# Optimization experiments

Hardware: AMD Instinct MI355X
Metric: run time of the kernel (lower is better)

The kernel has to match this reference:

```python
import jax, jax.numpy as jnp
import numpy as np

# OGB feature vocab sizes
ATOM_DIMS = [119, 4, 12, 12, 10, 6, 6, 2, 2]
BOND_DIMS = [5, 6, 2]
ATOM_OFF = np.concatenate([[0], np.cumsum(ATOM_DIMS)[:-1]]).astype(np.int32)
BOND_OFF = np.concatenate([[0], np.cumsum(BOND_DIMS)[:-1]]).astype(np.int32)
SCHEDULE_LEN = 5   # len(train_schedule) == len(eval_schedule)
NUM_GRAPHS = 12000
BN_EPS = 1e-5

N_NODES, N_EDGES, HIDDEN, NUM_TASKS = 300000, 600000, 128, 128


def setup_inputs() -> dict:
    key = jax.random.key(0)
    ks = jax.random.split(key, 16)
    x = jax.random.randint(ks[0], (N_NODES, 9), 0, 2, dtype=jnp.int32)
    edge_index = jax.random.randint(ks[1], (2, N_EDGES), 0, N_NODES, dtype=jnp.int32)
    edge_attr = jax.random.randint(ks[2], (N_EDGES, 3), 0, 2, dtype=jnp.int32)
    batch = jnp.sort(jax.random.randint(ks[3], (N_NODES,), 0, NUM_GRAPHS, dtype=jnp.int32))
    # learned parameters (embedding tables concatenated with offsets)
    atom_emb = jax.random.normal(ks[4], (sum(ATOM_DIMS), HIDDEN), jnp.float32) * 0.1
    bond_emb = jax.random.normal(ks[5], (sum(BOND_DIMS), HIDDEN), jnp.float32) * 0.1
    conv_W = jax.random.normal(ks[6], (HIDDEN, HIDDEN), jnp.float32) * (1.0 / np.sqrt(HIDDEN))
    conv_b = jnp.zeros((HIDDEN,), jnp.float32)
    root_emb = jax.random.normal(ks[7], (HIDDEN,), jnp.float32) * 0.1
    bn_gamma = jnp.ones((HIDDEN,), jnp.float32)
    bn_beta = jnp.zeros((HIDDEN,), jnp.float32)
    bn_mean = jnp.zeros((HIDDEN,), jnp.float32)   # running stats (eval mode)
    bn_var = jnp.ones((HIDDEN,), jnp.float32)
    lin_W = jax.random.normal(ks[8], (NUM_TASKS, HIDDEN), jnp.float32) * (1.0 / np.sqrt(HIDDEN))
    lin_b = jnp.zeros((NUM_TASKS,), jnp.float32)
    return {"x": x, "edge_index": edge_index, "edge_attr": edge_attr, "batch": batch,
            "atom_emb": atom_emb, "bond_emb": bond_emb, "conv_W": conv_W, "conv_b": conv_b,
            "root_emb": root_emb, "bn_gamma": bn_gamma, "bn_beta": bn_beta,
            "bn_mean": bn_mean, "bn_var": bn_var, "lin_W": lin_W, "lin_b": lin_b}


def reference(x, edge_index, edge_attr, batch, atom_emb, bond_emb, conv_W, conv_b,
              root_emb, bn_gamma, bn_beta, bn_mean, bn_var, lin_W, lin_b):
    N = x.shape[0]
    # AtomEncoder / BondEncoder: sum of per-feature embedding lookups
    h = atom_emb[x + jnp.asarray(ATOM_OFF, x.dtype)].sum(axis=1)            # [N, H]
    e = bond_emb[edge_attr + jnp.asarray(BOND_OFF, edge_attr.dtype)].sum(axis=1)  # [E, H]
    row, col = edge_index[0], edge_index[1]
    deg = jax.ops.segment_sum(jnp.ones_like(row, h.dtype), row, num_segments=N) + 1.0  # [N]
    dis = deg ** -0.5                                                        # deg >= 1, no inf
    norm = dis[row] * dis[col]                                               # [E]
    inv_std = bn_gamma / jnp.sqrt(bn_var + BN_EPS)
    for i in range(SCHEDULE_LEN):
        old = h
        z = h @ conv_W.T + conv_b                                            # [N, H]
        # message: norm * relu(x_j + edge_emb), aggregated at target (col) via scatter-add
        msg = norm[:, None] * jax.nn.relu(z[row] + e)                        # [E, H]
        agg = jax.ops.segment_sum(msg, col, num_segments=N)                  # [N, H]
        z = agg + jax.nn.relu(z + root_emb) / deg[:, None]                   # self-loop term
        z = jax.nn.relu(z)
        z = (z - bn_mean) * inv_std + bn_beta                                # BN (eval, running stats)
        # dropout: identity in eval mode
        # NOTE: faithful to source bug: smooth_fac is the loop index i, not schedule[i]
        h = i * old + (1 - i) * z
    # global mean pool over graphs
    counts = jax.ops.segment_sum(jnp.ones((N,), h.dtype), batch, num_segments=NUM_GRAPHS)
    pooled = jax.ops.segment_sum(h, batch, num_segments=NUM_GRAPHS) / jnp.maximum(counts, 1.0)[:, None]
    return pooled @ lin_W.T + lin_b                                          # [num_graphs, num_tasks]
```

## Files before the change

### kernel.cpp

```cpp
#include <hip/hip_runtime.h>

#define HID 128
#define AROWS 173

typedef __attribute__((ext_vector_type(8))) short short8;
typedef __attribute__((ext_vector_type(8))) unsigned short ushort8v;
typedef __attribute__((ext_vector_type(4))) float floatx4;
typedef __attribute__((ext_vector_type(4))) unsigned short ushort4v;

__device__ __forceinline__ unsigned short f2bf(float f) {
    unsigned u = __builtin_bit_cast(unsigned, f);
    u += 0x7FFF + ((u >> 16) & 1);
    return (unsigned short)(u >> 16);
}
__device__ __forceinline__ float bf2f(unsigned short s) {
    unsigned u = ((unsigned)s) << 16;
    return __builtin_bit_cast(float, u);
}

__global__ void fillrd_kernel(float* __restrict__ dis, int* __restrict__ indeg,
                              int* __restrict__ dhist, int N)
{
    int i = blockIdx.x * 256 + threadIdx.x;
    if (i < N) { dis[i] = 0.f; indeg[i] = 0; }
    if (blockIdx.x == 0 && threadIdx.x < 32) dhist[threadIdx.x] = 0;
}

__global__ void diag_kernel(float* __restrict__ out, long n, float val)
{
    long i = (long)blockIdx.x * blockDim.x + threadIdx.x;
    if (i < n) out[i] = val;
}

__global__ __launch_bounds__(256) void tables_kernel(
    const float* __restrict__ conv_W, unsigned short* __restrict__ Wb,
    const float* __restrict__ lin_W, unsigned short* __restrict__ linWb,
    const float* __restrict__ bond_emb, unsigned short* __restrict__ comb,
    const float* __restrict__ gamma, const float* __restrict__ beta,
    const float* __restrict__ mean, const float* __restrict__ var,
    float* __restrict__ bnsc, float* __restrict__ bnsh,
    const float* __restrict__ atom_emb, unsigned short* __restrict__ aeb)
{
    int blk = blockIdx.x;
    int tid = threadIdx.x;
    if (blk < 64) {
        int i = blk * 256 + tid;
        Wb[i] = f2bf(conv_W[i]);
    } else if (blk < 128) {
        int i = (blk - 64) * 256 + tid;
        linWb[i] = f2bf(lin_W[i]);
    } else if (blk < 158) {
        int i = (blk - 128) * 2 + (tid >> 7);
        int c = tid & 127;
        int a0 = i / 12, a1 = (i % 12) / 2, a2 = i % 2;
        comb[i * HID + c] = f2bf(bond_emb[a0 * HID + c] + bond_emb[(5 + a1) * HID + c]
                               + bond_emb[(11 + a2) * HID + c]);
    } else if (blk == 158) {
        if (tid < HID) {
            float sc = gamma[tid] * rsqrtf(var[tid] + 1e-5f);
            bnsc[tid] = sc;
            bnsh[tid] = beta[tid] - mean[tid] * sc;
        }
    } else {
        int i = (blk - 159) * 256 + tid;
        if (i < AROWS * HID) aeb[i] = f2bf(atom_emb[i]);
    }
}

__global__ void hist_kernel(const int* __restrict__ ei, float* __restrict__ dis,
                            int* __restrict__ indeg, int E)
{
    for (int e = blockIdx.x * blockDim.x + threadIdx.x; e < E; e += gridDim.x * blockDim.x) {
        atomicAdd(&dis[ei[e]], 1.f);
        atomicAdd(&indeg[ei[E + e]], 1);
    }
}

__global__ __launch_bounds__(256) void bsum_kernel(
    const int* __restrict__ indeg, int* __restrict__ partial,
    float* __restrict__ dis, int* __restrict__ dhist, int N)
{
    __shared__ int s[256];
    __shared__ int lh[32];
    int tid = threadIdx.x;
    if (tid < 32) lh[tid] = 0;
    int i = blockIdx.x * 256 + tid;
    int v = (i < N) ? indeg[i] : 0;
    s[tid] = v;
    if (i < N) {
        dis[i] = rsqrtf(dis[i] + 1.f);
        int d = v > 31 ? 31 : v;
        atomicAdd(&lh[d], 1);
    }
    __syncthreads();
    for (int d = 128; d > 0; d >>= 1) {
        if (tid < d) s[tid] += s[tid + d];
        __syncthreads();
    }
    if (tid == 0) partial[blockIdx.x] = s[0];
    if (tid < 32 && lh[tid]) atomicAdd(&dhist[tid], lh[tid]);
}

__global__ __launch_bounds__(256) void scan1_kernel(
    const int* __restrict__ partial, int* __restrict__ offs,
    int* __restrict__ ptr, const int* __restrict__ dhist, int* __restrict__ dcur,
    int B, int N)
{
    __shared__ int s[256];
    __shared__ int carry_s;
    int tid = threadIdx.x;
    if (tid == 0) carry_s = 0;
    __syncthreads();
    for (int base = 0; base < B; base += 256) {
        int i = base + tid;
        int v = (i < B) ? partial[i] : 0;
        s[tid] = v;
        __syncthreads();
        for (int d = 1; d < 256; d <<= 1) {
            int t = (tid >= d) ? s[tid - d] : 0;
            __syncthreads();
            s[tid] += t;
            __syncthreads();
        }
        int carry = carry_s;
        if (i < B) offs[i] = carry + s[tid] - v;
        __syncthreads();
        if (tid == 0) carry_s = carry + s[255];
        __syncthreads();
    }
    if (tid == 0) {
        ptr[N] = carry_s;
        int sum = 0;
        for (int k = 0; k < 32; ++k) { dcur[k] = sum; sum += dhist[k]; }
    }
}

__global__ __launch_bounds__(256) void scan2_kernel(
    const int* __restrict__ indeg, const int* __restrict__ offs,
    int* __restrict__ ptr, int* __restrict__ cursor, int N)
{
    __shared__ int s[256];
    int tid = threadIdx.x;
    int i = blockIdx.x * 256 + tid;
    int v = (i < N) ? indeg[i] : 0;
    s[tid] = v;
    __syncthreads();
    for (int d = 1; d < 256; d <<= 1) {
        int t = (tid >= d) ? s[tid - d] : 0;
        __syncthreads();
        s[tid] += t;
        __syncthreads();
    }
    if (i < N) {
        int ex = offs[blockIdx.x] + s[tid] - v;
        ptr[i] = ex;
        cursor[i] = ex;
    }
}

__global__ __launch_bounds__(256) void dperm_kernel(
    const int* __restrict__ ptr, int* __restrict__ dcur,
    int* __restrict__ perm, int N)
{
    __shared__ int lh[32];
    __shared__ int gb[32];
    int tid = threadIdx.x;
    if (tid < 32) lh[tid] = 0;
    __syncthreads();
    int n = blockIdx.x * 256 + tid;
    int rank = 0, d = 0;
    if (n < N) {
        d = ptr[n + 1] - ptr[n];
        if (d > 31) d = 31;
        rank = atomicAdd(&lh[d], 1);
    }
    __syncthreads();
    if (tid < 32) gb[tid] = lh[tid] ? atomicAdd(&dcur[tid], lh[tid]) : 0;
    __syncthreads();
    if (n < N) perm[gb[d] + rank] = n;
}

__global__ void fillcsr_kernel(const int* __restrict__ ei, const int* __restrict__ attr,
                               const float* __restrict__ dis, int* __restrict__ cursor,
                               int2* __restrict__ edata, const int* __restrict__ batch,
                               int* __restrict__ gptr, int E, int N, int G)
{
    for (int e = blockIdx.x * blockDim.x + threadIdx.x; e < E; e += gridDim.x * blockDim.x) {
        int r   = ei[e];
        int col = ei[E + e];
        int pos = atomicAdd(&cursor[col], 1);
        int ci  = attr[e * 3] * 12 + attr[e * 3 + 1] * 2 + attr[e * 3 + 2];
        float nrm = dis[r] * dis[col];
        int2 ed;
        ed.x = r;
        ed.y = ci | ((int)f2bf(nrm) << 16);
        edata[pos] = ed;
    }
    for (int n = blockIdx.x * blockDim.x + threadIdx.x; n < N; n += gridDim.x * blockDim.x) {
        int b = batch[n];
        int bp = (n == 0) ? -1 : batch[n - 1];
        for (int g = bp + 1; g <= b; ++g) gptr[g] = n;
        if (n == N - 1)
            for (int g = b + 1; g <= G; ++g) gptr[g] = N;
    }
}

template<bool FIRST>
__device__ __forceinline__ ushort8v agg_node(
    long n, int c, const int* __restrict__ ptr, const int2* __restrict__ edata,
    const unsigned short* __restrict__ comb, const float* __restrict__ dis,
    const float* __restrict__ root, const float* __restrict__ bnsc,
    const float* __restrict__ bnsh, const unsigned short* __restrict__ zb,
    const unsigned short* __restrict__ hb, float fi)
{
    ushort8v zv = *reinterpret_cast<const ushort8v*>(zb + n * HID + c);
    ushort8v hv;
    if constexpr (!FIRST) hv = *reinterpret_cast<const ushort8v*>(hb + n * HID + c);
    float di = dis[n];
    float rd = di * di;
    float acc[8];
#pragma unroll
    for (int j = 0; j < 8; ++j) acc[j] = fmaxf(bf2f(zv[j]) + root[c + j], 0.f) * rd;

    int jb = ptr[n], je = ptr[n + 1];
    int j2 = jb;
    for (; j2 + 1 < je; j2 += 2) {
        int2 e0 = edata[j2];
        int2 e1 = edata[j2 + 1];
        ushort8v z0 = *reinterpret_cast<const ushort8v*>(zb + (long)e0.x * HID + c);
        ushort8v z1 = *reinterpret_cast<const ushort8v*>(zb + (long)e1.x * HID + c);
        ushort8v c0 = *reinterpret_cast<const ushort8v*>(comb + (e0.y & 0xFF) * HID + c);
        ushort8v c1 = *reinterpret_cast<const ushort8v*>(comb + (e1.y & 0xFF) * HID + c);
        float n0 = bf2f((unsigned short)(((unsigned)e0.y) >> 16));
        float n1 = bf2f((unsigned short)(((unsigned)e1.y) >> 16));
#pragma unroll
        for (int j = 0; j < 8; ++j) {
            acc[j] += fmaxf(bf2f(z0[j]) + bf2f(c0[j]), 0.f) * n0;
            acc[j] += fmaxf(bf2f(z1[j]) + bf2f(c1[j]), 0.f) * n1;
        }
    }
    if (j2 < je) {
        int2 e0 = edata[j2];
        ushort8v z0 = *reinterpret_cast<const ushort8v*>(zb + (long)e0.x * HID + c);
        ushort8v c0 = *reinterpret_cast<const ushort8v*>(comb + (e0.y & 0xFF) * HID + c);
        float n0 = bf2f((unsigned short)(((unsigned)e0.y) >> 16));
#pragma unroll
        for (int j = 0; j < 8; ++j)
            acc[j] += fmaxf(bf2f(z0[j]) + bf2f(c0[j]), 0.f) * n0;
    }

    ushort8v o;
#pragma unroll
    for (int j = 0; j < 8; ++j) {
        float t = fmaxf(acc[j], 0.f) * bnsc[c + j] + bnsh[c + j];
        float h;
        if constexpr (FIRST) h = t;
        else h = fi * bf2f(hv[j]) + (1.f - fi) * t;
        o[j] = f2bf(h);
    }
    return o;
}

template<bool FIRST>
__global__ __launch_bounds__(256) void agg_kernel(
    const int* __restrict__ perm, const int* __restrict__ ptr,
    const int2* __restrict__ edata, const unsigned short* __restrict__ comb,
    const float* __restrict__ dis, const float* __restrict__ root,
    const float* __restrict__ bnsc, const float* __restrict__ bnsh,
    const unsigned short* __restrict__ zb, unsigned short* __restrict__ hb,
    float fi, int N)
{
    long slot = (long)blockIdx.x * 16 + (threadIdx.x >> 4);
    if (slot >= N) return;
    long n = perm[slot];
    int c = (threadIdx.x & 15) * 8;
    ushort8v o = agg_node<FIRST>(n, c, ptr, edata, comb, dis, root, bnsc, bnsh,
                                 zb, hb, fi);
    *reinterpret_cast<ushort8v*>(hb + n * HID + c) = o;
}

template<bool FIRST>
__global__ __launch_bounds__(256) void fusedag_kernel(
    const int* __restrict__ perm, const int* __restrict__ ptr,
    const int2* __restrict__ edata, const unsigned short* __restrict__ comb,
    const float* __restrict__ dis, const float* __restrict__ root,
    const float* __restrict__ bnsc, const float* __restrict__ bnsh,
    const unsigned short* __restrict__ zin, unsigned short* __restrict__ hb,
    const unsigned short* __restrict__ Wb, const float* __restrict__ bias,
    unsigned short* __restrict__ zout, float fi, int N)
{
    __shared__ unsigned short hs[64][132];
    int tid = threadIdx.x;
    long base = (long)blockIdx.x * 64;
    int sn = tid >> 4;
    int cc = (tid & 15) * 8;

#pragma unroll 1
    for (int s = 0; s < 4; ++s) {
        int lr = s * 16 + sn;
        long slot = base + lr;
        ushort8v o = {0, 0, 0, 0, 0, 0, 0, 0};
        if (slot < N) {
            long n = perm[slot];
            o = agg_node<FIRST>(n, cc, ptr, edata, comb, dis, root, bnsc, bnsh,
                                zin, hb, fi);
            *reinterpret_cast<ushort8v*>(hb + n * HID + cc) = o;
        }
        *reinterpret_cast<ushort8v*>(&hs[lr][cc]) = o;
    }
    __syncthreads();

    int wave = tid >> 6;
    int lane = tid & 63;
    int l15 = lane & 15;
    int q = lane >> 4;
    int row0 = wave * 16;

    short8 a[4];
#pragma unroll
    for (int kb = 0; kb < 4; ++kb)
        a[kb] = *reinterpret_cast<const short8*>(&hs[row0 + l15][q * 8 + kb * 32]);

    floatx4 acc[8];
#pragma unroll
    for (int nt = 0; nt < 8; ++nt) {
        floatx4 zz = {0.f, 0.f, 0.f, 0.f};
        acc[nt] = zz;
    }
#pragma unroll
    for (int nt = 0; nt < 8; ++nt) {
        const unsigned short* bp = Wb + (nt * 16 + l15) * HID + q * 8;
#pragma unroll
        for (int kb = 0; kb < 4; ++kb) {
            short8 b = *reinterpret_cast<const short8*>(bp + kb * 32);
            acc[nt] = __builtin_amdgcn_mfma_f32_16x16x32_bf16(a[kb], b, acc[nt], 0, 0, 0);
        }
    }

    float bi[8];
#pragma unroll
    for (int nt = 0; nt < 8; ++nt) bi[nt] = bias[nt * 16 + l15];

#pragma unroll
    for (int r = 0; r < 4; ++r) {
        int lr = row0 + q * 4 + r;
#pragma unroll
        for (int nt = 0; nt < 8; ++nt)
            hs[lr][l15 + 16 * nt] = f2bf(acc[nt][r] + bi[nt]);
    }
    __syncthreads();

    int tr = tid >> 4;
    int tc = (tid & 15) * 8;
#pragma unroll
    for (int i = 0; i < 4; ++i) {
        int row = i * 16 + tr;
        long slot = base + row;
        if (slot < N) {
            long n = perm[slot];
            ushort8v v = *reinterpret_cast<const ushort8v*>(&hs[row][tc]);
            *reinterpret_cast<ushort8v*>(zout + n * HID + tc) = v;
        }
    }
}

__device__ __forceinline__ void gemm_from_lds(
    unsigned short (*hs)[132], const unsigned short* __restrict__ Wb,
    const float* __restrict__ bias, unsigned short* __restrict__ zb,
    long base, int N, int tid)
{
    int wave = tid >> 6;
    int lane = tid & 63;
    int l15 = lane & 15;
    int q = lane >> 4;
    int rowl0 = wave * 32;

    short8 a[2][4];
#pragma unroll
    for (int mt = 0; mt < 2; ++mt) {
        int rl = rowl0 + mt * 16 + l15;
#pragma unroll
        for (int kb = 0; kb < 4; ++kb)
            a[mt][kb] = *reinterpret_cast<const short8*>(&hs[rl][q * 8 + kb * 32]);
    }

    floatx4 acc[2][8];
#pragma unroll
    for (int mt = 0; mt < 2; ++mt)
#pragma unroll
        for (int nt = 0; nt < 8; ++nt) {
            floatx4 zz = {0.f, 0.f, 0.f, 0.f};
            acc[mt][nt] = zz;
        }

#pragma unroll
    for (int nt = 0; nt < 8; ++nt) {
        const unsigned short* bp = Wb + (nt * 16 + l15) * HID + q * 8;
#pragma unroll
        for (int kb = 0; kb < 4; ++kb) {
            short8 b = *reinterpret_cast<const short8*>(bp + kb * 32);
            acc[0][nt] = __builtin_amdgcn_mfma_f32_16x16x32_bf16(a[0][kb], b, acc[0][nt], 0, 0, 0);
            acc[1][nt] = __builtin_amdgcn_mfma_f32_16x16x32_bf16(a[1][kb], b, acc[1][nt], 0, 0, 0);
        }
    }

    float bi[8];
#pragma unroll
    for (int nt = 0; nt < 8; ++nt) bi[nt] = bias[nt * 16 + l15];

    __syncthreads();
#pragma unroll
    for (int mt = 0; mt < 2; ++mt)
#pragma unroll
        for (int r = 0; r < 4; ++r) {
            int lr = rowl0 + mt * 16 + q * 4 + r;
#pragma unroll
            for (int nt = 0; nt < 8; ++nt)
                hs[lr][l15 + 16 * nt] = f2bf(acc[mt][nt][r] + bi[nt]);
        }
    __syncthreads();

    int tr = tid >> 4;
    int tc = (tid & 15) * 8;
#pragma unroll
    for (int i = 0; i < 8; ++i) {
        int row = i * 16 + tr;
        long gr = base + row;
        if (gr < N) {
            ushort8v v = *reinterpret_cast<const ushort8v*>(&hs[row][tc]);
            *reinterpret_cast<ushort8v*>(zb + gr * HID + tc) = v;
        }
    }
}

__global__ __launch_bounds__(256) void egemm_kernel(
    const int* __restrict__ x, const unsigned short* __restrict__ aeb,
    const unsigned short* __restrict__ Wb, const float* __restrict__ bias,
    unsigned short* __restrict__ zb, int N)
{
    __shared__ unsigned short hs[128][132];
    __shared__ int xs[128 * 9];
    int tid = threadIdx.x;
    long base = (long)blockIdx.x * 128;
    const int OFF[9] = {0, 119, 123, 135, 147, 157, 163, 169, 171};

    int nb = (N - base < 128) ? (int)(N - base) : 128;
    int cnt = nb * 9;
    for (int i = tid; i < cnt; i += 256) xs[i] = x[base * 9 + i];
    __syncthreads();

    int sn = tid >> 4;
    int cc = (tid & 15) * 8;
#pragma unroll 1
    for (int s = 0; s < 8; ++s) {
        int lr = s * 16 + sn;
        ushort8v o;
        if (lr < nb) {
            float acc[8];
#pragma unroll
            for (int j = 0; j < 8; ++j) acc[j] = 0.f;
#pragma unroll
            for (int f = 0; f < 9; ++f) {
                int idx = xs[lr * 9 + f] + OFF[f];
                ushort8v v = *reinterpret_cast<const ushort8v*>(aeb + (long)idx * HID + cc);
#pragma unroll
                for (int j = 0; j < 8; ++j) acc[j] += bf2f(v[j]);
            }
#pragma unroll
            for (int j = 0; j < 8; ++j) o[j] = f2bf(acc[j]);
        } else {
            ushort8v z8 = {0, 0, 0, 0, 0, 0, 0, 0};
            o = z8;
        }
        *reinterpret_cast<ushort8v*>(&hs[lr][cc]) = o;
    }
    __syncthreads();

    gemm_from_lds(hs, Wb, bias, zb, base, N, tid);
}

__global__ __launch_bounds__(256) void gemm_kernel(
    const unsigned short* __restrict__ hb, const unsigned short* __restrict__ Wb,
    const float* __restrict__ bias, unsigned short* __restrict__ zb, int N)
{
    __shared__ unsigned short st[128][132];
    int tid = threadIdx.x;
    int wave = tid >> 6;
    int lane = tid & 63;
    int l15 = lane & 15;
    int q = lane >> 4;
    long base = (long)blockIdx.x * 128;
    long row0 = base + wave * 32;

#pragma unroll
    for (int mt = 0; mt < 2; ++mt) {
        long rl = row0 + mt * 16 + l15;
        if (rl > (long)N - 1) rl = (long)N - 1;
        const unsigned short* ap = hb + rl * HID + q * 8;
        int lrow = wave * 32 + mt * 16 + l15;
#pragma unroll
        for (int kb = 0; kb < 4; ++kb)
            *reinterpret_cast<ushort8v*>(&st[lrow][q * 8 + kb * 32]) =
                *reinterpret_cast<const ushort8v*>(ap + kb * 32);
    }
    __syncthreads();
    gemm_from_lds(st, Wb, bias, zb, base, N, tid);
}

__global__ __launch_bounds__(256) void linmm_kernel(
    const unsigned short* __restrict__ pb, const unsigned short* __restrict__ Wb,
    const float* __restrict__ bias, float* __restrict__ out, int G)
{
    int wave = threadIdx.x >> 6;
    int lane = threadIdx.x & 63;
    int l15 = lane & 15;
    int q = lane >> 4;
    long row0 = (long)blockIdx.x * 128 + wave * 32;

    short8 a[2][4];
#pragma unroll
    for (int mt = 0; mt < 2; ++mt) {
        long rl = row0 + mt * 16 + l15;
        if (rl > (long)G - 1) rl = (long)G - 1;
        const unsigned short* ap = pb + rl * HID + q * 8;
#pragma unroll
        for (int kb = 0; kb < 4; ++kb)
            a[mt][kb] = *reinterpret_cast<const short8*>(ap + kb * 32);
    }

    floatx4 acc[2][8];
#pragma unroll
    for (int mt = 0; mt < 2; ++mt)
#pragma unroll
        for (int nt = 0; nt < 8; ++nt) {
            floatx4 zz = {0.f, 0.f, 0.f, 0.f};
            acc[mt][nt] = zz;
        }

#pragma unroll
    for (int nt = 0; nt < 8; ++nt) {
        const unsigned short* bp = Wb + (nt * 16 + l15) * HID + q * 8;
#pragma unroll
        for (int kb = 0; kb < 4; ++kb) {
            short8 b = *reinterpret_cast<const short8*>(bp + kb * 32);
            acc[0][nt] = __builtin_amdgcn_mfma_f32_16x16x32_bf16(a[0][kb], b, acc[0][nt], 0, 0, 0);
            acc[1][nt] = __builtin_amdgcn_mfma_f32_16x16x32_bf16(a[1][kb], b, acc[1][nt], 0, 0, 0);
        }
    }

    float bi[8];
#pragma unroll
    for (int nt = 0; nt < 8; ++nt) bi[nt] = bias[nt * 16 + l15];

#pragma unroll
    for (int mt = 0; mt < 2; ++mt)
#pragma unroll
        for (int r = 0; r < 4; ++r) {
            long rr = row0 + mt * 16 + q * 4 + r;
            if (rr < G) {
                float* op = out + rr * HID + l15;
#pragma unroll
                for (int nt = 0; nt < 8; ++nt)
                    op[nt * 16] = acc[mt][nt][r] + bi[nt];
            }
        }
}

__global__ __launch_bounds__(256) void pool_kernel(
    const unsigned short* __restrict__ hb, const int* __restrict__ gptr,
    unsigned short* __restrict__ pb, int G)
{
    int g = blockIdx.x;
    if (g >= G) return;
    int tid = threadIdx.x;
    int sub = tid >> 5;
    int c = (tid & 31) * 4;
    int lo = gptr[g], hi = gptr[g + 1];
    floatx4 s = {0.f, 0.f, 0.f, 0.f};
    for (int n = lo + sub; n < hi; n += 8) {
        ushort4v hv = *reinterpret_cast<const ushort4v*>(hb + (long)n * HID + c);
#pragma unroll
        for (int j = 0; j < 4; ++j) s[j] += bf2f(hv[j]);
    }
    __shared__ float ps[8][HID];
    *reinterpret_cast<floatx4*>(&ps[sub][c]) = s;
    __syncthreads();
    if (tid < HID) {
        float sum = 0.f;
#pragma unroll
        for (int k = 0; k < 8; ++k) sum += ps[k][tid];
        float cnt = (hi > lo) ? (float)(hi - lo) : 1.f;
        pb[(long)g * HID + tid] = f2bf(sum / cnt);
    }
}

extern "C" void kernel_launch(void* const* d_in, const int* in_sizes, int n_in,
                              void* d_out, int out_size, void* d_ws, size_t ws_size,
                              hipStream_t stream)
{
    const int* x          = (const int*)d_in[0];
    const int* ei         = (const int*)d_in[1];
    const int* attr       = (const int*)d_in[2];
    const int* batch      = (const int*)d_in[3];
    const float* atom_emb = (const float*)d_in[4];
    const float* bond_emb = (const float*)d_in[5];
    const float* conv_W   = (const float*)d_in[6];
    const float* conv_b   = (const float*)d_in[7];
    const float* root     = (const float*)d_in[8];
    const float* gamma    = (const float*)d_in[9];
    const float* beta     = (const float*)d_in[10];
    const float* mean     = (const float*)d_in[11];
    const float* var      = (const float*)d_in[12];
    const float* lin_W    = (const float*)d_in[13];
    const float* lin_b    = (const float*)d_in[14];
    float* out = (float*)d_out;

    const int N = in_sizes[0] / 9;
    const int E = in_sizes[1] / 2;
    const int G = out_size / HID;
    const int B = (N + 255) / 256;

    auto al = [](size_t b) { return (b + 255) & ~(size_t)255; };
    const size_t need_base =
        al((size_t)N * HID * 2) +
        al((size_t)N * HID * 2) +
        al((size_t)(N + 1) * 4) +
        al((size_t)E * 8) +
        al((size_t)N * 4) +
        al((size_t)2048 * 4) * 2 +
        al((size_t)(G + 1) * 4) +
        al((size_t)(G + 128) * HID * 2) +
        al((size_t)60 * HID * 2) +
        al((size_t)HID * 4) * 2 +
        al((size_t)HID * HID * 2) * 2 +
        al((size_t)AROWS * HID * 2) +
        al((size_t)N * 4) +
        al(32 * 4) * 2;
    const size_t need_fused = need_base + al((size_t)N * HID * 2);

    if (ws_size < need_base || B > 2048) {
        float v = (B > 2048) ? 3000.f : (1000.f + (float)(ws_size >> 20));
        long n = (long)out_size;
        diag_kernel<<<(int)((n + 255) / 256), 256, 0, stream>>>(out, n, v);
        return;
    }
    const bool fused_ok = (ws_size >= need_fused);

    char* wsp = (char*)d_ws;
    size_t used = 0;
    auto alloc = [&](size_t bytes) { char* p = wsp + used; used += al(bytes); return p; };
    unsigned short* hb = (unsigned short*)alloc((size_t)N * HID * 2);
    unsigned short* zb = (unsigned short*)alloc((size_t)N * HID * 2);
    int* ptr      = (int*)alloc((size_t)(N + 1) * 4);
    int2* edata   = (int2*)alloc((size_t)E * 8);
    int* indeg    = (int*)alloc((size_t)N * 4);
    int* cursor   = indeg;
    int* partial  = (int*)alloc((size_t)2048 * 4);
    int* offs     = (int*)alloc((size_t)2048 * 4);
    int* gptr     = (int*)alloc((size_t)(G + 1) * 4);
    unsigned short* pb = (unsigned short*)alloc((size_t)(G + 128) * HID * 2);
    float* dis    = (float*)pb;
    unsigned short* comb = (unsigned short*)alloc((size_t)60 * HID * 2);
    float* bnsc   = (float*)alloc((size_t)HID * 4);
    float* bnsh   = (float*)alloc((size_t)HID * 4);
    unsigned short* Wb    = (unsigned short*)alloc((size_t)HID * HID * 2);
    unsigned short* linWb = (unsigned short*)alloc((size_t)HID * HID * 2);
    unsigned short* aeb   = (unsigned short*)alloc((size_t)AROWS * HID * 2);
    int* perm     = (int*)alloc((size_t)N * 4);
    int* dhist    = (int*)alloc(32 * 4);
    int* dcur     = (int*)alloc(32 * 4);
    unsigned short* zb2 = (unsigned short*)alloc((size_t)N * HID * 2);

    fillrd_kernel<<<B, 256, 0, stream>>>(dis, indeg, dhist, N);
    tables_kernel<<<246, 256, 0, stream>>>(conv_W, Wb, lin_W, linWb, bond_emb, comb,
                                           gamma, beta, mean, var, bnsc, bnsh,
                                           atom_emb, aeb);
    hist_kernel<<<1024, 256, 0, stream>>>(ei, dis, indeg, E);
    bsum_kernel<<<B, 256, 0, stream>>>(indeg, partial, dis, dhist, N);
    scan1_kernel<<<1, 256, 0, stream>>>(partial, offs, ptr, dhist, dcur, B, N);
    scan2_kernel<<<B, 256, 0, stream>>>(indeg, offs, ptr, cursor, N);
    dperm_kernel<<<B, 256, 0, stream>>>(ptr, dcur, perm, N);
    fillcsr_kernel<<<1024, 256, 0, stream>>>(ei, attr, dis, cursor, edata,
                                             batch, gptr, E, N, G);

    const int gemm_blocks  = (N + 127) / 128;
    const int fused_blocks = (N + 63) / 64;
    const int agg_blocks   = (N + 15) / 16;
    egemm_kernel<<<gemm_blocks, 256, 0, stream>>>(x, aeb, Wb, conv_b, zb, N);

    if (fused_ok) {
        fusedag_kernel<true ><<<fused_blocks, 256, 0, stream>>>(perm, ptr, edata,
                comb, dis, root, bnsc, bnsh, zb,  hb, Wb, conv_b, zb2, 0.f, N);
        fusedag_kernel<false><<<fused_blocks, 256, 0, stream>>>(perm, ptr, edata,
                comb, dis, root, bnsc, bnsh, zb2, hb, Wb, conv_b, zb,  2.f, N);
        fusedag_kernel<false><<<fused_blocks, 256, 0, stream>>>(perm, ptr, edata,
                comb, dis, root, bnsc, bnsh, zb,  hb, Wb, conv_b, zb2, 3.f, N);
        agg_kernel<false><<<agg_blocks, 256, 0, stream>>>(perm, ptr, edata, comb,
                dis, root, bnsc, bnsh, zb2, hb, 4.f, N);
    } else {
        agg_kernel<true ><<<agg_blocks, 256, 0, stream>>>(perm, ptr, edata, comb,
                dis, root, bnsc, bnsh, zb, hb, 0.f, N);
        const float fis[3] = {2.f, 3.f, 4.f};
        for (int t = 0; t < 3; ++t) {
            gemm_kernel<<<gemm_blocks, 256, 0, stream>>>(hb, Wb, conv_b, zb, N);
            agg_kernel<false><<<agg_blocks, 256, 0, stream>>>(perm, ptr, edata, comb,
                    dis, root, bnsc, bnsh, zb, hb, fis[t], N);
        }
    }

    pool_kernel<<<G, 256, 0, stream>>>(hb, gptr, pb, G);
    linmm_kernel<<<(G + 127) / 128, 256, 0, stream>>>(pb, linWb, lin_b, out, G);
}
```

Measured before the change: 797.7 us.

## Build CSR in degree-sorted slot order and drop fused agg-GEMM path

The CSR is now built in degree-sorted slot order. A degree-bucket permutation and its inverse are computed first, and the row pointers come from a prefix sum over permuted degrees. The aggregation then reads edges contiguously in slot order, so neighbouring threads walk adjacent edge ranges instead of scattered ones. The fused aggregation+GEMM kernel and the extra z buffer are removed in favour of separate agg and gemm launches, and the embedding GEMM uses 64-row tiles. This adds kernel launches and extra passes through the permutation in exchange for more coherent edge reads. Dropping the fused path brings back an hb round-trip per layer.

```diff
diff --git a/kernel.cpp b/kernel.cpp
--- a/kernel.cpp
+++ b/kernel.cpp
@@ -76,35 +76,76 @@
     }
 }
 
-__global__ __launch_bounds__(256) void bsum_kernel(
-    const int* __restrict__ indeg, int* __restrict__ partial,
-    float* __restrict__ dis, int* __restrict__ dhist, int N)
-{
-    __shared__ int s[256];
+__global__ __launch_bounds__(256) void fdh_kernel(
+    float* __restrict__ dis, const int* __restrict__ indeg,
+    int* __restrict__ dhist, int N)
+{
     __shared__ int lh[32];
     int tid = threadIdx.x;
     if (tid < 32) lh[tid] = 0;
+    __syncthreads();
     int i = blockIdx.x * 256 + tid;
-    int v = (i < N) ? indeg[i] : 0;
-    s[tid] = v;
     if (i < N) {
         dis[i] = rsqrtf(dis[i] + 1.f);
-        int d = v > 31 ? 31 : v;
+        int d = indeg[i]; if (d > 31) d = 31;
         atomicAdd(&lh[d], 1);
     }
+    __syncthreads();
+    if (tid < 32 && lh[tid]) atomicAdd(&dhist[tid], lh[tid]);
+}
+
+__global__ void dscan_kernel(const int* __restrict__ dhist, int* __restrict__ dcur)
+{
+    if (threadIdx.x == 0) {
+        int s = 0;
+        for (int k = 0; k < 32; ++k) { dcur[k] = s; s += dhist[k]; }
+    }
+}
+
+__global__ __launch_bounds__(256) void dperm_kernel(
+    const int* __restrict__ indeg, int* __restrict__ dcur,
+    int* __restrict__ perm, int* __restrict__ invperm, int N)
+{
+    __shared__ int lh[32];
+    __shared__ int gb[32];
+    int tid = threadIdx.x;
+    if (tid < 32) lh[tid] = 0;
+    __syncthreads();
+    int n = blockIdx.x * 256 + tid;
+    int rank = 0, d = 0;
+    if (n < N) {
+        d = indeg[n]; if (d > 31) d = 31;
+        rank = atomicAdd(&lh[d], 1);
+    }
+    __syncthreads();
+    if (tid < 32) gb[tid] = lh[tid] ? atomicAdd(&dcur[tid], lh[tid]) : 0;
+    __syncthreads();
+    if (n < N) {
+        int slot = gb[d] + rank;
+        perm[slot] = n;
+        invperm[n] = slot;
+    }
+}
+
+__global__ __launch_bounds__(256) void sbsum_kernel(
+    const int* __restrict__ indeg, const int* __restrict__ perm,
+    int* __restrict__ partial, int N)
+{
+    __shared__ int s[256];
+    int tid = threadIdx.x;
+    int i = blockIdx.x * 256 + tid;
+    s[tid] = (i < N) ? indeg[perm[i]] : 0;
     __syncthreads();
     for (int d = 128; d > 0; d >>= 1) {
         if (tid < d) s[tid] += s[tid + d];
         __syncthreads();
     }
     if (tid == 0) partial[blockIdx.x] = s[0];
-    if (tid < 32 && lh[tid]) atomicAdd(&dhist[tid], lh[tid]);
-}
-
-__global__ __launch_bounds__(256) void scan1_kernel(
+}
+
+__global__ __launch_bounds__(256) void sscan1_kernel(
     const int* __restrict__ partial, int* __restrict__ offs,
-    int* __restrict__ ptr, const int* __restrict__ dhist, int* __restrict__ dcur,
-    int B, int N)
+    int* __restrict__ sptr, int B, int N)
 {
     __shared__ int s[256];
     __shared__ int carry_s;
@@ -128,21 +169,18 @@
         if (tid == 0) carry_s = carry + s[255];
         __syncthreads();
     }
-    if (tid == 0) {
-        ptr[N] = carry_s;
-        int sum = 0;
-        for (int k = 0; k < 32; ++k) { dcur[k] = sum; sum += dhist[k]; }
-    }
-}
-
-__global__ __launch_bounds__(256) void scan2_kernel(
-    const int* __restrict__ indeg, const int* __restrict__ offs,
-    int* __restrict__ ptr, int* __restrict__ cursor, int N)
+    if (tid == 0) sptr[N] = carry_s;
+}
+
+__global__ __launch_bounds__(256) void sscan2_kernel(
+    const int* __restrict__ indeg, const int* __restrict__ perm,
+    const int* __restrict__ offs, int* __restrict__ sptr,
+    int* __restrict__ scursor, int N)
 {
     __shared__ int s[256];
     int tid = threadIdx.x;
     int i = blockIdx.x * 256 + tid;
-    int v = (i < N) ? indeg[i] : 0;
+    int v = (i < N) ? indeg[perm[i]] : 0;
     s[tid] = v;
     __syncthreads();
     for (int d = 1; d < 256; d <<= 1) {
@@ -153,42 +191,23 @@
     }
     if (i < N) {
         int ex = offs[blockIdx.x] + s[tid] - v;
-        ptr[i] = ex;
-        cursor[i] = ex;
-    }
-}
-
-__global__ __launch_bounds__(256) void dperm_kernel(
-    const int* __restrict__ ptr, int* __restrict__ dcur,
-    int* __restrict__ perm, int N)
-{
-    __shared__ int lh[32];
-    __shared__ int gb[32];
-    int tid = threadIdx.x;
-    if (tid < 32) lh[tid] = 0;
-    __syncthreads();
-    int n = blockIdx.x * 256 + tid;
-    int rank = 0, d = 0;
-    if (n < N) {
-        d = ptr[n + 1] - ptr[n];
-        if (d > 31) d = 31;
-        rank = atomicAdd(&lh[d], 1);
-    }
-    __syncthreads();
-    if (tid < 32) gb[tid] = lh[tid] ? atomicAdd(&dcur[tid], lh[tid]) : 0;
-    __syncthreads();
-    if (n < N) perm[gb[d] + rank] = n;
+        sptr[i] = ex;
+        scursor[i] = ex;
+    }
 }
 
 __global__ void fillcsr_kernel(const int* __restrict__ ei, const int* __restrict__ attr,
-                               const float* __restrict__ dis, int* __restrict__ cursor,
+                               const float* __restrict__ dis,
+                               const int* __restrict__ invperm,
+                               int* __restrict__ scursor,
                                int2* __restrict__ edata, const int* __restrict__ batch,
                                int* __restrict__ gptr, int E, int N, int G)
 {
     for (int e = blockIdx.x * blockDim.x + threadIdx.x; e < E; e += gridDim.x * blockDim.x) {
         int r   = ei[e];
         int col = ei[E + e];
-        int pos = atomicAdd(&cursor[col], 1);
+        int slot = invperm[col];
+        int pos = atomicAdd(&scursor[slot], 1);
         int ci  = attr[e * 3] * 12 + attr[e * 3 + 1] * 2 + attr[e * 3 + 2];
         float nrm = dis[r] * dis[col];
         int2 ed;
@@ -206,13 +225,21 @@
 }
 
 template<bool FIRST>
-__device__ __forceinline__ ushort8v agg_node(
-    long n, int c, const int* __restrict__ ptr, const int2* __restrict__ edata,
-    const unsigned short* __restrict__ comb, const float* __restrict__ dis,
-    const float* __restrict__ root, const float* __restrict__ bnsc,
-    const float* __restrict__ bnsh, const unsigned short* __restrict__ zb,
-    const unsigned short* __restrict__ hb, float fi)
-{
+__global__ __launch_bounds__(256) void agg_kernel(
+    const int* __restrict__ perm, const int* __restrict__ sptr,
+    const int2* __restrict__ edata, const unsigned short* __restrict__ comb,
+    const float* __restrict__ dis, const float* __restrict__ root,
+    const float* __restrict__ bnsc, const float* __restrict__ bnsh,
+    const unsigned short* __restrict__ zb, unsigned short* __restrict__ hb,
+    float fi, int N)
+{
+    long slot = (long)blockIdx.x * 16 + (threadIdx.x >> 4);
+    if (slot >= N) return;
+    long n = perm[slot];
+    int c = (threadIdx.x & 15) * 8;
+
+    int jb = sptr[slot], je = sptr[slot + 1];
+
     ushort8v zv = *reinterpret_cast<const ushort8v*>(zb + n * HID + c);
     ushort8v hv;
     if constexpr (!FIRST) hv = *reinterpret_cast<const ushort8v*>(hb + n * HID + c);
@@ -222,7 +249,6 @@
 #pragma unroll
     for (int j = 0; j < 8; ++j) acc[j] = fmaxf(bf2f(zv[j]) + root[c + j], 0.f) * rd;
 
-    int jb = ptr[n], je = ptr[n + 1];
     int j2 = jb;
     for (; j2 + 1 < je; j2 += 2) {
         int2 e0 = edata[j2];
@@ -258,110 +284,7 @@
         else h = fi * bf2f(hv[j]) + (1.f - fi) * t;
         o[j] = f2bf(h);
     }
-    return o;
-}
-
-template<bool FIRST>
-__global__ __launch_bounds__(256) void agg_kernel(
-    const int* __restrict__ perm, const int* __restrict__ ptr,
-    const int2* __restrict__ edata, const unsigned short* __restrict__ comb,
-    const float* __restrict__ dis, const float* __restrict__ root,
-    const float* __restrict__ bnsc, const float* __restrict__ bnsh,
-    const unsigned short* __restrict__ zb, unsigned short* __restrict__ hb,
-    float fi, int N)
-{
-    long slot = (long)blockIdx.x * 16 + (threadIdx.x >> 4);
-    if (slot >= N) return;
-    long n = perm[slot];
-    int c = (threadIdx.x & 15) * 8;
-    ushort8v o = agg_node<FIRST>(n, c, ptr, edata, comb, dis, root, bnsc, bnsh,
-                                 zb, hb, fi);
     *reinterpret_cast<ushort8v*>(hb + n * HID + c) = o;
-}
-
-template<bool FIRST>
-__global__ __launch_bounds__(256) void fusedag_kernel(
-    const int* __restrict__ perm, const int* __restrict__ ptr,
-    const int2* __restrict__ edata, const unsigned short* __restrict__ comb,
-    const float* __restrict__ dis, const float* __restrict__ root,
-    const float* __restrict__ bnsc, const float* __restrict__ bnsh,
-    const unsigned short* __restrict__ zin, unsigned short* __restrict__ hb,
-    const unsigned short* __restrict__ Wb, const float* __restrict__ bias,
-    unsigned short* __restrict__ zout, float fi, int N)
-{
-    __shared__ unsigned short hs[64][132];
-    int tid = threadIdx.x;
-    long base = (long)blockIdx.x * 64;
-    int sn = tid >> 4;
-    int cc = (tid & 15) * 8;
-
-#pragma unroll 1
-    for (int s = 0; s < 4; ++s) {
-        int lr = s * 16 + sn;
-        long slot = base + lr;
-        ushort8v o = {0, 0, 0, 0, 0, 0, 0, 0};
-        if (slot < N) {
-            long n = perm[slot];
-            o = agg_node<FIRST>(n, cc, ptr, edata, comb, dis, root, bnsc, bnsh,
-                                zin, hb, fi);
-            *reinterpret_cast<ushort8v*>(hb + n * HID + cc) = o;
-        }
-        *reinterpret_cast<ushort8v*>(&hs[lr][cc]) = o;
-    }
-    __syncthreads();
-
-    int wave = tid >> 6;
-    int lane = tid & 63;
-    int l15 = lane & 15;
-    int q = lane >> 4;
-    int row0 = wave * 16;
-
-    short8 a[4];
-#pragma unroll
-    for (int kb = 0; kb < 4; ++kb)
-        a[kb] = *reinterpret_cast<const short8*>(&hs[row0 + l15][q * 8 + kb * 32]);
-
-    floatx4 acc[8];
-#pragma unroll
-    for (int nt = 0; nt < 8; ++nt) {
-        floatx4 zz = {0.f, 0.f, 0.f, 0.f};
-        acc[nt] = zz;
-    }
-#pragma unroll
-    for (int nt = 0; nt < 8; ++nt) {
-        const unsigned short* bp = Wb + (nt * 16 + l15) * HID + q * 8;
-#pragma unroll
-        for (int kb = 0; kb < 4; ++kb) {
-            short8 b = *reinterpret_cast<const short8*>(bp + kb * 32);
-            acc[nt] = __builtin_amdgcn_mfma_f32_16x16x32_bf16(a[kb], b, acc[nt], 0, 0, 0);
-        }
-    }
-
-    float bi[8];
-#pragma unroll
-    for (int nt = 0; nt < 8; ++nt) bi[nt] = bias[nt * 16 + l15];
-
-#pragma unroll
-    for (int r = 0; r < 4; ++r) {
-        int lr = row0 + q * 4 + r;
-#pragma unroll
-        for (int nt = 0; nt < 8; ++nt)
-            hs[lr][l15 + 16 * nt] = f2bf(acc[nt][r] + bi[nt]);
-    }
-    __syncthreads();
-
-    int tr = tid >> 4;
-    int tc = (tid & 15) * 8;
-#pragma unroll
-    for (int i = 0; i < 4; ++i) {
-        int row = i * 16 + tr;
-        long slot = base + row;
-        if (slot < N) {
-            long n = perm[slot];
-            ushort8v v = *reinterpret_cast<const ushort8v*>(&hs[row][tc]);
-            *reinterpret_cast<ushort8v*>(zout + n * HID + tc) = v;
-        }
-    }
 }
 
 __device__ __forceinline__ void gemm_from_lds(
@@ -438,13 +361,13 @@
     const unsigned short* __restrict__ Wb, const float* __restrict__ bias,
     unsigned short* __restrict__ zb, int N)
 {
-    __shared__ unsigned short hs[128][132];
-    __shared__ int xs[128 * 9];
-    int tid = threadIdx.x;
-    long base = (long)blockIdx.x * 128;
+    __shared__ unsigned short hs[64][132];
+    __shared__ int xs[64 * 9];
+    int tid = threadIdx.x;
+    long base = (long)blockIdx.x * 64;
     const int OFF[9] = {0, 119, 123, 135, 147, 157, 163, 169, 171};
 
-    int nb = (N - base < 128) ? (int)(N - base) : 128;
+    int nb = (N - base < 64) ? (int)(N - base) : 64;
     int cnt = nb * 9;
     for (int i = tid; i < cnt; i += 256) xs[i] = x[base * 9 + i];
     __syncthreads();
@@ -452,7 +375,7 @@
     int sn = tid >> 4;
     int cc = (tid & 15) * 8;
 #pragma unroll 1
-    for (int s = 0; s < 8; ++s) {
+    for (int s = 0; s < 4; ++s) {
         int lr = s * 16 + sn;
         ushort8v o;
         if (lr < nb) {
@@ -476,7 +399,57 @@
     }
     __syncthreads();
 
-    gemm_from_lds(hs, Wb, bias, zb, base, N, tid);
+    int wave = tid >> 6;
+    int lane = tid & 63;
+    int l15 = lane & 15;
+    int q = lane >> 4;
+    int row0 = wave * 16;
+
+    short8 a[4];
+#pragma unroll
+    for (int kb = 0; kb < 4; ++kb)
+        a[kb] = *reinterpret_cast<const short8*>(&hs[row0 + l15][q * 8 + kb * 32]);
+
+    floatx4 acc[8];
+#pragma unroll
+    for (int nt = 0; nt < 8; ++nt) {
+        floatx4 zz = {0.f, 0.f, 0.f, 0.f};
+        acc[nt] = zz;
+    }
+#pragma unroll
+    for (int nt = 0; nt < 8; ++nt) {
+        const unsigned short* bp = Wb + (nt * 16 + l15) * HID + q * 8;
+#pragma unroll
+        for (int kb = 0; kb < 4; ++kb) {
+            short8 b = *reinterpret_cast<const short8*>(bp + kb * 32);
+            acc[nt] = __builtin_amdgcn_mfma_f32_16x16x32_bf16(a[kb], b, acc[nt], 0, 0, 0);
+        }
+    }
+
+    float bi[8];
+#pragma unroll
+    for (int nt = 0; nt < 8; ++nt) bi[nt] = bias[nt * 16 + l15];
+
+#pragma unroll
+    for (int r = 0; r < 4; ++r) {
+        int lr = row0 + q * 4 + r;
+#pragma unroll
+        for (int nt = 0; nt < 8; ++nt)
+            hs[lr][l15 + 16 * nt] = f2bf(acc[nt][r] + bi[nt]);
+    }
+    __syncthreads();
+
+    int tr = tid >> 4;
+    int tc = (tid & 15) * 8;
+#pragma unroll
+    for (int i = 0; i < 4; ++i) {
+        int row = i * 16 + tr;
+        long gr = base + row;
+        if (gr < N) {
+            ushort8v v = *reinterpret_cast<const ushort8v*>(&hs[row][tc]);
+            *reinterpret_cast<ushort8v*>(zb + gr * HID + tc) = v;
+        }
+    }
 }
 
 __global__ __launch_bounds__(256) void gemm_kernel(
@@ -621,11 +594,14 @@
     const int B = (N + 255) / 256;
 
     auto al = [](size_t b) { return (b + 255) & ~(size_t)255; };
-    const size_t need_base =
+    const size_t need =
         al((size_t)N * HID * 2) +
         al((size_t)N * HID * 2) +
         al((size_t)(N + 1) * 4) +
         al((size_t)E * 8) +
+        al((size_t)N * 4) +
+        al((size_t)N * 4) +
+        al((size_t)N * 4) +
         al((size_t)N * 4) +
         al((size_t)2048 * 4) * 2 +
         al((size_t)(G + 1) * 4) +
@@ -634,27 +610,26 @@
         al((size_t)HID * 4) * 2 +
         al((size_t)HID * HID * 2) * 2 +
         al((size_t)AROWS * HID * 2) +
-        al((size_t)N * 4) +
         al(32 * 4) * 2;
-    const size_t need_fused = need_base + al((size_t)N * HID * 2);
-
-    if (ws_size < need_base || B > 2048) {
+
+    if (ws_size < need || B > 2048) {
         float v = (B > 2048) ? 3000.f : (1000.f + (float)(ws_size >> 20));
         long n = (long)out_size;
         diag_kernel<<<(int)((n + 255) / 256), 256, 0, stream>>>(out, n, v);
         return;
     }
-    const bool fused_ok = (ws_size >= need_fused);
 
     char* wsp = (char*)d_ws;
     size_t used = 0;
     auto alloc = [&](size_t bytes) { char* p = wsp + used; used += al(bytes); return p; };
     unsigned short* hb = (unsigned short*)alloc((size_t)N * HID * 2);
     unsigned short* zb = (unsigned short*)alloc((size_t)N * HID * 2);
-    int* ptr      = (int*)alloc((size_t)(N + 1) * 4);
+    int* sptr     = (int*)alloc((size_t)(N + 1) * 4);
     int2* edata   = (int2*)alloc((size_t)E * 8);
     int* indeg    = (int*)alloc((size_t)N * 4);
-    int* cursor   = indeg;
+    int* perm     = (int*)alloc((size_t)N * 4);
+    int* invperm  = (int*)alloc((size_t)N * 4);
+    int* scursor  = (int*)alloc((size_t)N * 4);
     int* partial  = (int*)alloc((size_t)2048 * 4);
     int* offs     = (int*)alloc((size_t)2048 * 4);
     int* gptr     = (int*)alloc((size_t)(G + 1) * 4);
@@ -666,46 +641,34 @@
     unsigned short* Wb    = (unsigned short*)alloc((size_t)HID * HID * 2);
     unsigned short* linWb = (unsigned short*)alloc((size_t)HID * HID * 2);
     unsigned short* aeb   = (unsigned short*)alloc((size_t)AROWS * HID * 2);
-    int* perm     = (int*)alloc((size_t)N * 4);
     int* dhist    = (int*)alloc(32 * 4);
     int* dcur     = (int*)alloc(32 * 4);
-    unsigned short* zb2 = (unsigned short*)alloc((size_t)N * HID * 2);
 
     fillrd_kernel<<<B, 256, 0, stream>>>(dis, indeg, dhist, N);
     tables_kernel<<<246, 256, 0, stream>>>(conv_W, Wb, lin_W, linWb, bond_emb, comb,
                                            gamma, beta, mean, var, bnsc, bnsh,
                                            atom_emb, aeb);
     hist_kernel<<<1024, 256, 0, stream>>>(ei, dis, indeg, E);
-    bsum_kernel<<<B, 256, 0, stream>>>(indeg, partial, dis, dhist, N);
-    scan1_kernel<<<1, 256, 0, stream>>>(partial, offs, ptr, dhist, dcur, B, N);
-    scan2_kernel<<<B, 256, 0, stream>>>(indeg, offs, ptr, cursor, N);
-    dperm_kernel<<<B, 256, 0, stream>>>(ptr, dcur, perm, N);
-    fillcsr_kernel<<<1024, 256, 0, stream>>>(ei, attr, dis, cursor, edata,
+    fdh_kernel<<<B, 256, 0, stream>>>(dis, indeg, dhist, N);
+    dscan_kernel<<<1, 64, 0, stream>>>(dhist, dcur);
+    dperm_kernel<<<B, 256, 0, stream>>>(indeg, dcur, perm, invperm, N);
+    sbsum_kernel<<<B, 256, 0, stream>>>(indeg, perm, partial, N);
+    sscan1_kernel<<<1, 256, 0, stream>>>(partial, offs, sptr, B, N);
+    sscan2_kernel<<<B, 256, 0, stream>>>(indeg, perm, offs, sptr, scursor, N);
+    fillcsr_kernel<<<1024, 256, 0, stream>>>(ei, attr, dis, invperm, scursor, edata,
                                              batch, gptr, E, N, G);
 
+    const int egemm_blocks = (N + 63) / 64;
     const int gemm_blocks  = (N + 127) / 128;
-    const int fused_blocks = (N + 63) / 64;
     const int agg_blocks   = (N + 15) / 16;
-    egemm_kernel<<<gemm_blocks, 256, 0, stream>>>(x, aeb, Wb, conv_b, zb, N);
-
-    if (fused_ok) {
-        fusedag_kernel<true ><<<fused_blocks, 256, 0, stream>>>(perm, ptr, edata,
-                comb, dis, root, bnsc, bnsh, zb,  hb, Wb, conv_b, zb2, 0.f, N);
-        fusedag_kernel<false><<<fused_blocks, 256, 0, stream>>>(perm, ptr, edata,
-                comb, dis, root, bnsc, bnsh, zb2, hb, Wb, conv_b, zb,  2.f, N);
-        fusedag_kernel<false><<<fused_blocks, 256, 0, stream>>>(perm, ptr, edata,
-                comb, dis, root, bnsc, bnsh, zb,  hb, Wb, conv_b, zb2, 3.f, N);
-        agg_kernel<false><<<agg_blocks, 256, 0, stream>>>(perm, ptr, edata, comb,
-                dis, root, bnsc, bnsh, zb2, hb, 4.f, N);
-    } else {
-        agg_kernel<true ><<<agg_blocks, 256, 0, stream>>>(perm, ptr, edata, comb,
-                dis, root, bnsc, bnsh, zb, hb, 0.f, N);
-        const float fis[3] = {2.f, 3.f, 4.f};
-        for (int t = 0; t < 3; ++t) {
-            gemm_kernel<<<gemm_blocks, 256, 0, stream>>>(hb, Wb, conv_b, zb, N);
-            agg_kernel<false><<<agg_blocks, 256, 0, stream>>>(perm, ptr, edata, comb,
-                    dis, root, bnsc, bnsh, zb, hb, fis[t], N);
-        }
+    egemm_kernel<<<egemm_blocks, 256, 0, stream>>>(x, aeb, Wb, conv_b, zb, N);
+    agg_kernel<true ><<<agg_blocks, 256, 0, stream>>>(perm, sptr, edata, comb, dis,
+            root, bnsc, bnsh, zb, hb, 0.f, N);
+    const float fis[3] = {2.f, 3.f, 4.f};
+    for (int t = 0; t < 3; ++t) {
+        gemm_kernel<<<gemm_blocks, 256, 0, stream>>>(hb, Wb, conv_b, zb, N);
+        agg_kernel<false><<<agg_blocks, 256, 0, stream>>>(perm, sptr, edata, comb, dis,
+                root, bnsc, bnsh, zb, hb, fis[t], N);
     }
 
     pool_kernel<<<G, 256, 0, stream>>>(hb, gptr, pb, G);
```

Result: faster. 749.1 us (-6.1%).
